# Kernel tuning notes

Measured on AMD Instinct MI355X. Metric: run time of the kernel, lower is better.

The kernel has to match this reference:

```python
import jax, jax.numpy as jnp
import numpy as np

N_NODES = 100000
N_EDGES = 3200000
IN_FEATS = 128
OUT_FEATS = 16
NEG_SLOPE = 0.2


def setup_inputs() -> dict:
    key = jax.random.key(0)
    k1, k2, k3, k4, k5, k6 = jax.random.split(key, 6)
    h = jax.random.normal(k1, (N_NODES, IN_FEATS), dtype=jnp.float32)
    src = jax.random.randint(k2, (N_EDGES,), 0, N_NODES, dtype=jnp.int64)
    dst = jax.random.randint(k3, (N_EDGES,), 0, N_NODES, dtype=jnp.int64)
    W = jax.random.normal(k4, (OUT_FEATS, IN_FEATS), dtype=jnp.float32) * (1.0 / np.sqrt(IN_FEATS))
    a_l = jax.random.normal(k5, (1, OUT_FEATS), dtype=jnp.float32) * (1.0 / np.sqrt(OUT_FEATS))
    a_r = jax.random.normal(k6, (1, OUT_FEATS), dtype=jnp.float32) * (1.0 / np.sqrt(OUT_FEATS))
    return {"h": h, "src": src, "dst": dst, "W": W, "a_l": a_l, "a_r": a_r}


def reference(h, src, dst, W, a_l, a_r):
    N = h.shape[0]
    # node projection: h @ fc.weight.T  -> [N, out]
    hW = h @ W.T
    # per-node attention logits: [N, 1]
    el = hW @ a_l.T
    er = hW @ a_r.T
    # u_add_v: per-edge logit e = el[src] + er[dst], then leaky_relu(0.2)
    e = jax.nn.leaky_relu(el[src] + er[dst], negative_slope=NEG_SLOPE)  # [E, 1]
    # edge_softmax over edges grouped by destination node (numerically stable)
    emax = jax.ops.segment_max(e, dst, num_segments=N)  # [N, 1], -inf for empty
    emax = jnp.where(jnp.isfinite(emax), emax, 0.0)
    e_exp = jnp.exp(e - emax[dst])
    esum = jax.ops.segment_sum(e_exp, dst, num_segments=N)  # [N, 1]
    alpha = e_exp / jnp.maximum(esum[dst], 1e-16)  # [E, 1]
    # u_mul_e + sum: weighted aggregation of source features at destinations
    out = jax.ops.segment_sum(hW[src] * alpha, dst, num_segments=N)  # [N, out]
    return out
```

## Files before the change

kernel.cpp:

```cpp
#include <hip/hip_runtime.h>
#include <hip/hip_bf16.h>
#include <stdint.h>

#define IN_F 128
#define OUT_F 16
#define NEG_SLOPE 0.2f
#define SB_BITS 9
#define SB_NODES 512
#define NBS 196
#define CAP_SB 17408
#define TILE_NODES 128
#define LCAP 4608
#define SC_E 8192
#define SB_SPACING 200

#define SMEM_BYTES (3136 + SC_E * 4)

__global__ __launch_bounds__(256) void proj_scatter_kernel(
    const float* __restrict__ h, const float* __restrict__ W,
    const float* __restrict__ a_l, const float* __restrict__ a_r,
    const int* __restrict__ src, const int* __restrict__ dst,
    __hip_bfloat16* __restrict__ hWbf, float* __restrict__ el,
    float* __restrict__ er, int* __restrict__ cursor,
    uint32_t* __restrict__ payload, int N, int E, int scatBlocks) {
  __shared__ __align__(16) uint8_t smem[SMEM_BYTES];
  int t = threadIdx.x;

  if ((int)blockIdx.x < scatBlocks) {
    int* hist = (int*)smem;
    int* pref = hist + NBS;
    int* gbase = pref + NBS;
    int* rank = gbase + NBS;
    uint32_t* sortedP = (uint32_t*)(smem + 3136);

    int start = blockIdx.x * SC_E;
    int end = min(E, start + SC_E);
    int cnt = end - start;

    if (t < NBS) { hist[t] = 0; rank[t] = 0; }
    __syncthreads();

    const int4* d4 = (const int4*)(dst + start);
    int n4 = cnt >> 2;
    for (int i = t; i < n4; i += 256) {
      int4 d = d4[i];
      atomicAdd(&hist[d.x >> SB_BITS], 1);
      atomicAdd(&hist[d.y >> SB_BITS], 1);
      atomicAdd(&hist[d.z >> SB_BITS], 1);
      atomicAdd(&hist[d.w >> SB_BITS], 1);
    }
    for (int i = start + (n4 << 2) + t; i < end; i += 256)
      atomicAdd(&hist[dst[i] >> SB_BITS], 1);
    __syncthreads();

    if (t < NBS) {
      int s = 0;
      for (int j = 0; j < t; ++j) s += hist[j];
      pref[t] = s;
      int c = hist[t];
      gbase[t] = c ? atomicAdd(&cursor[t * 16], c) : 0;
    }
    __syncthreads();

    const int4* s4 = (const int4*)(src + start);
    for (int i = t; i < n4; i += 256) {
      int4 d = d4[i];
      int4 s = s4[i];
#pragma unroll
      for (int j = 0; j < 4; ++j) {
        int dd = j == 0 ? d.x : j == 1 ? d.y : j == 2 ? d.z : d.w;
        int ss = j == 0 ? s.x : j == 1 ? s.y : j == 2 ? s.z : s.w;
        int b = dd >> SB_BITS;
        int r = atomicAdd(&rank[b], 1);
        sortedP[pref[b] + r] =
            ((uint32_t)ss << SB_BITS) | (uint32_t)(dd & (SB_NODES - 1));
      }
    }
    for (int i = start + (n4 << 2) + t; i < end; i += 256) {
      int dd = dst[i];
      int b = dd >> SB_BITS;
      int r = atomicAdd(&rank[b], 1);
      sortedP[pref[b] + r] =
          ((uint32_t)src[i] << SB_BITS) | (uint32_t)(dd & (SB_NODES - 1));
    }
    __syncthreads();

    int wv = t >> 6, ln = t & 63;
    for (int b = wv; b < NBS; b += 4) {
      int c = hist[b];
      int p0 = pref[b];
      size_t g0 = (size_t)b * CAP_SB + gbase[b];
      for (int j = ln; j < c; j += 64)
        if (gbase[b] + j < CAP_SB) payload[g0 + j] = sortedP[p0 + j];
    }
  } else {
    float* Ws = (float*)smem;
    for (int i = t; i < OUT_F * IN_F; i += 256) Ws[i] = W[i];
    __syncthreads();

    int node = ((int)blockIdx.x - scatBlocks) * 256 + t;
    if (node >= N) return;

    const float4* hrow = (const float4*)(h + (size_t)node * IN_F);
    float acc[OUT_F];
#pragma unroll
    for (int f = 0; f < OUT_F; ++f) acc[f] = 0.f;

#pragma unroll 4
    for (int k = 0; k < IN_F / 4; ++k) {
      float4 hv = hrow[k];
#pragma unroll
      for (int f = 0; f < OUT_F; ++f) {
        float4 wv = ((const float4*)(Ws + f * IN_F))[k];
        acc[f] += hv.x * wv.x + hv.y * wv.y + hv.z * wv.z + hv.w * wv.w;
      }
    }

    union {
      unsigned short us[OUT_F];
      uint4 q[2];
    } pk;
#pragma unroll
    for (int f = 0; f < OUT_F; ++f) {
      __hip_bfloat16 b = __float2bfloat16(acc[f]);
      pk.us[f] = *reinterpret_cast<unsigned short*>(&b);
    }
    uint4* dstq = (uint4*)(hWbf + (size_t)node * OUT_F);
    dstq[0] = pk.q[0];
    dstq[1] = pk.q[1];

    float vl = 0.f, vr = 0.f;
#pragma unroll
    for (int f = 0; f < OUT_F; ++f) {
      vl += acc[f] * a_l[f];
      vr += acc[f] * a_r[f];
    }
    el[node] = vl;
    er[node] = vr;
  }
}

__global__ __launch_bounds__(512) void agg_kernel(
    const uint32_t* __restrict__ payload, const int* __restrict__ cursor,
    const __hip_bfloat16* __restrict__ hWbf, const float* __restrict__ el,
    const float* __restrict__ er, float* __restrict__ out, int N) {
  __shared__ uint32_t sorted[LCAP];
  __shared__ float exS[LCAP];
  __shared__ int hist[TILE_NODES];
  __shared__ int pref[TILE_NODES];
  __shared__ int rank[TILE_NODES];
  __shared__ int kcnt;
  uint32_t* kept = (uint32_t*)exS;

  int t = threadIdx.x;
  int sb = blockIdx.x % SB_SPACING;
  uint32_t quad = blockIdx.x / SB_SPACING;
  if (sb >= NBS) return;
  size_t base = (size_t)sb * CAP_SB;
  int cnt = min(cursor[sb * 16], CAP_SB);

  if (t < TILE_NODES) { hist[t] = 0; rank[t] = 0; }
  if (t == 0) kcnt = 0;
  __syncthreads();

  const uint4* pay4 = (const uint4*)(payload + base);
  int n4 = (cnt + 3) >> 2;
  int lane = t & 63;
  for (int i = t; i < n4; i += 512) {
    uint4 v = pay4[i];
    int i0 = i << 2;
#pragma unroll
    for (int j = 0; j < 4; ++j) {
      uint32_t p = j == 0 ? v.x : j == 1 ? v.y : j == 2 ? v.z : v.w;
      bool keep = (i0 + j < cnt) && (((p >> 7) & 3u) == quad);
      unsigned long long m = __ballot(keep);
      if (m) {
        int leader = (int)(__ffsll((long long)m) - 1);
        int bbase = 0;
        if (lane == leader) bbase = atomicAdd(&kcnt, (int)__popcll(m));
        bbase = __shfl(bbase, leader);
        if (keep)
          kept[bbase + (int)__popcll(m & ((1ull << lane) - 1))] = p;
      }
    }
  }
  __syncthreads();
  int K = min(kcnt, LCAP);

  for (int i = t; i < K; i += 512)
    atomicAdd(&hist[kept[i] & (TILE_NODES - 1)], 1);
  __syncthreads();

  if (t < TILE_NODES) {
    int s = 0;
    for (int j = 0; j < t; ++j) s += hist[j];
    pref[t] = s;
  }
  __syncthreads();

  for (int i = t; i < K; i += 512) {
    uint32_t p = kept[i];
    int dl = (int)(p & (TILE_NODES - 1));
    int r = atomicAdd(&rank[dl], 1);
    sorted[pref[dl] + r] = p;
  }
  __syncthreads();

  int node0 = sb * SB_NODES + (int)quad * TILE_NODES;
  for (int i = t; i < K; i += 512) {
    uint32_t p = sorted[i];
    int s = (int)(p >> SB_BITS);
    float x = el[s] + er[node0 + (int)(p & (TILE_NODES - 1))];
    x = x > 0.f ? x : NEG_SLOPE * x;
    exS[i] = __expf(x);
  }
  __syncthreads();

  int g = t >> 4;
  int f = t & 15;
  for (int dl = g; dl < TILE_NODES; dl += 32) {
    int node = node0 + dl;
    if (node >= N) break;
    int k = pref[dl];
    int kend = k + hist[dl];
    float acc = 0.f;
    float es = 0.f;
#pragma unroll 4
    for (; k < kend; ++k) {
      float ex = exS[k];
      acc += ex * __bfloat162float(hWbf[(int)(sorted[k] >> SB_BITS) * OUT_F + f]);
      es += ex;
    }
    out[(size_t)node * OUT_F + f] = acc / fmaxf(es, 1e-16f);
  }
}

extern "C" void kernel_launch(void* const* d_in, const int* in_sizes, int n_in,
                              void* d_out, int out_size, void* d_ws, size_t ws_size,
                              hipStream_t stream) {
  const float* h   = (const float*)d_in[0];
  const int*   src = (const int*)d_in[1];
  const int*   dst = (const int*)d_in[2];
  const float* W   = (const float*)d_in[3];
  const float* a_l = (const float*)d_in[4];
  const float* a_r = (const float*)d_in[5];
  float* out = (float*)d_out;

  const int N = in_sizes[0] / IN_F;
  const int E = in_sizes[1];
  const int scatBlocks = (E + SC_E - 1) / SC_E;
  const int projBlocks = (N + 255) / 256;

  __hip_bfloat16* hWbf = (__hip_bfloat16*)d_ws;
  float* el = (float*)(hWbf + (size_t)N * OUT_F);
  float* er = el + N;
  int* cursor = (int*)(er + N);
  uint32_t* payload = (uint32_t*)(cursor + (size_t)NBS * 16);

  hipMemsetAsync(cursor, 0, (size_t)NBS * 16 * sizeof(int), stream);

  proj_scatter_kernel<<<scatBlocks + projBlocks, 256, 0, stream>>>(
      h, W, a_l, a_r, src, dst, hWbf, el, er, cursor, payload, N, E, scatBlocks);

  agg_kernel<<<SB_SPACING * 4, 512, 0, stream>>>(payload, cursor, hWbf, el, er,
                                                 out, N);
}
```

Before: 184.1 us.

## Bucket edges directly into 128-node tiles and vectorize aggregation gathers

The scatter pass now bins edges into 782 buckets of 128 destination nodes instead of 196 superbuckets of 512. Each aggregation block therefore reads only its own edges and no longer scans four times the payload with ballot-based filtering. The aggregation stage assigns 4 threads per node, each loading 4 bf16 features as a uint2 and writing a float4 output. The cost is more buckets in the scatter histogram and prefix scan (now two-level), smaller and more scattered payload write segments, and a fixed per-bucket capacity that could overflow on skewed inputs.

```diff
diff --git a/kernel.cpp b/kernel.cpp
--- a/kernel.cpp
+++ b/kernel.cpp
@@ -5,16 +5,19 @@
 #define IN_F 128
 #define OUT_F 16
 #define NEG_SLOPE 0.2f
-#define SB_BITS 9
-#define SB_NODES 512
-#define NBS 196
-#define CAP_SB 17408
-#define TILE_NODES 128
-#define LCAP 4608
+#define LB_BITS 7
+#define LB_NODES 128
+#define NB 782
+#define CAP 4608
 #define SC_E 8192
-#define SB_SPACING 200
-
-#define SMEM_BYTES (3136 + SC_E * 4)
+
+#define SMEM_BYTES (12512 + 1024 + SC_E * 4)
+
+__device__ __forceinline__ float u2f(uint32_t u) {
+  union { uint32_t i; float f; } c;
+  c.i = u;
+  return c.f;
+}
 
 __global__ __launch_bounds__(256) void proj_scatter_kernel(
     const float* __restrict__ h, const float* __restrict__ W,
@@ -28,37 +31,56 @@
 
   if ((int)blockIdx.x < scatBlocks) {
     int* hist = (int*)smem;
-    int* pref = hist + NBS;
-    int* gbase = pref + NBS;
-    int* rank = gbase + NBS;
-    uint32_t* sortedP = (uint32_t*)(smem + 3136);
+    int* pref = hist + NB;
+    int* gbase = pref + NB;
+    int* rank = gbase + NB;
+    int* tsum = rank + NB;
+    uint32_t* sortedP = (uint32_t*)(tsum + 256);
 
     int start = blockIdx.x * SC_E;
     int end = min(E, start + SC_E);
     int cnt = end - start;
 
-    if (t < NBS) { hist[t] = 0; rank[t] = 0; }
+    for (int i = t; i < NB; i += 256) { hist[i] = 0; rank[i] = 0; }
     __syncthreads();
 
     const int4* d4 = (const int4*)(dst + start);
     int n4 = cnt >> 2;
     for (int i = t; i < n4; i += 256) {
       int4 d = d4[i];
-      atomicAdd(&hist[d.x >> SB_BITS], 1);
-      atomicAdd(&hist[d.y >> SB_BITS], 1);
-      atomicAdd(&hist[d.z >> SB_BITS], 1);
-      atomicAdd(&hist[d.w >> SB_BITS], 1);
+      atomicAdd(&hist[d.x >> LB_BITS], 1);
+      atomicAdd(&hist[d.y >> LB_BITS], 1);
+      atomicAdd(&hist[d.z >> LB_BITS], 1);
+      atomicAdd(&hist[d.w >> LB_BITS], 1);
     }
     for (int i = start + (n4 << 2) + t; i < end; i += 256)
-      atomicAdd(&hist[dst[i] >> SB_BITS], 1);
-    __syncthreads();
-
-    if (t < NBS) {
-      int s = 0;
-      for (int j = 0; j < t; ++j) s += hist[j];
-      pref[t] = s;
-      int c = hist[t];
-      gbase[t] = c ? atomicAdd(&cursor[t * 16], c) : 0;
+      atomicAdd(&hist[dst[i] >> LB_BITS], 1);
+    __syncthreads();
+
+    {
+      int b0 = t * 4;
+      int s_loc = 0;
+      if (b0 < NB) {
+        int lim = min(b0 + 4, NB);
+        for (int j = b0; j < lim; ++j) s_loc += hist[j];
+      }
+      tsum[t] = s_loc;
+    }
+    __syncthreads();
+    {
+      int pre = 0;
+      for (int j = 0; j < t; ++j) pre += tsum[j];
+      int b0 = t * 4;
+      if (b0 < NB) {
+        int lim = min(b0 + 4, NB);
+        int run = pre;
+        for (int j = b0; j < lim; ++j) {
+          pref[j] = run;
+          int c = hist[j];
+          run += c;
+          gbase[j] = c ? atomicAdd(&cursor[j * 16], c) : 0;
+        }
+      }
     }
     __syncthreads();
 
@@ -70,28 +92,30 @@
       for (int j = 0; j < 4; ++j) {
         int dd = j == 0 ? d.x : j == 1 ? d.y : j == 2 ? d.z : d.w;
         int ss = j == 0 ? s.x : j == 1 ? s.y : j == 2 ? s.z : s.w;
-        int b = dd >> SB_BITS;
+        int b = dd >> LB_BITS;
         int r = atomicAdd(&rank[b], 1);
         sortedP[pref[b] + r] =
-            ((uint32_t)ss << SB_BITS) | (uint32_t)(dd & (SB_NODES - 1));
+            ((uint32_t)ss << LB_BITS) | (uint32_t)(dd & (LB_NODES - 1));
       }
     }
     for (int i = start + (n4 << 2) + t; i < end; i += 256) {
       int dd = dst[i];
-      int b = dd >> SB_BITS;
+      int b = dd >> LB_BITS;
       int r = atomicAdd(&rank[b], 1);
       sortedP[pref[b] + r] =
-          ((uint32_t)src[i] << SB_BITS) | (uint32_t)(dd & (SB_NODES - 1));
-    }
-    __syncthreads();
-
-    int wv = t >> 6, ln = t & 63;
-    for (int b = wv; b < NBS; b += 4) {
+          ((uint32_t)src[i] << LB_BITS) | (uint32_t)(dd & (LB_NODES - 1));
+    }
+    __syncthreads();
+
+    int g16 = t >> 4, l16 = t & 15;
+    for (int b = g16; b < NB; b += 16) {
       int c = hist[b];
+      if (c == 0) continue;
       int p0 = pref[b];
-      size_t g0 = (size_t)b * CAP_SB + gbase[b];
-      for (int j = ln; j < c; j += 64)
-        if (gbase[b] + j < CAP_SB) payload[g0 + j] = sortedP[p0 + j];
+      int gb = gbase[b];
+      size_t g0 = (size_t)b * CAP + (size_t)gb;
+      for (int j = l16; j < c; j += 16)
+        if (gb + j < CAP) payload[g0 + j] = sortedP[p0 + j];
     }
   } else {
     float* Ws = (float*)smem;
@@ -144,94 +168,80 @@
     const uint32_t* __restrict__ payload, const int* __restrict__ cursor,
     const __hip_bfloat16* __restrict__ hWbf, const float* __restrict__ el,
     const float* __restrict__ er, float* __restrict__ out, int N) {
-  __shared__ uint32_t sorted[LCAP];
-  __shared__ float exS[LCAP];
-  __shared__ int hist[TILE_NODES];
-  __shared__ int pref[TILE_NODES];
-  __shared__ int rank[TILE_NODES];
-  __shared__ int kcnt;
+  __shared__ __align__(16) uint32_t sorted[CAP];
+  __shared__ __align__(16) float exS[CAP];
+  __shared__ int hist[LB_NODES];
+  __shared__ int pref[LB_NODES];
+  __shared__ int rank[LB_NODES];
   uint32_t* kept = (uint32_t*)exS;
 
   int t = threadIdx.x;
-  int sb = blockIdx.x % SB_SPACING;
-  uint32_t quad = blockIdx.x / SB_SPACING;
-  if (sb >= NBS) return;
-  size_t base = (size_t)sb * CAP_SB;
-  int cnt = min(cursor[sb * 16], CAP_SB);
-
-  if (t < TILE_NODES) { hist[t] = 0; rank[t] = 0; }
-  if (t == 0) kcnt = 0;
+  int b = blockIdx.x;
+  size_t base = (size_t)b * CAP;
+  int cnt = min(cursor[b * 16], CAP);
+  int node0 = b << LB_BITS;
+
+  if (t < LB_NODES) { hist[t] = 0; rank[t] = 0; }
   __syncthreads();
 
   const uint4* pay4 = (const uint4*)(payload + base);
+  uint4* kept4 = (uint4*)kept;
   int n4 = (cnt + 3) >> 2;
-  int lane = t & 63;
   for (int i = t; i < n4; i += 512) {
     uint4 v = pay4[i];
+    kept4[i] = v;
     int i0 = i << 2;
-#pragma unroll
-    for (int j = 0; j < 4; ++j) {
-      uint32_t p = j == 0 ? v.x : j == 1 ? v.y : j == 2 ? v.z : v.w;
-      bool keep = (i0 + j < cnt) && (((p >> 7) & 3u) == quad);
-      unsigned long long m = __ballot(keep);
-      if (m) {
-        int leader = (int)(__ffsll((long long)m) - 1);
-        int bbase = 0;
-        if (lane == leader) bbase = atomicAdd(&kcnt, (int)__popcll(m));
-        bbase = __shfl(bbase, leader);
-        if (keep)
-          kept[bbase + (int)__popcll(m & ((1ull << lane) - 1))] = p;
-      }
-    }
-  }
-  __syncthreads();
-  int K = min(kcnt, LCAP);
-
-  for (int i = t; i < K; i += 512)
-    atomicAdd(&hist[kept[i] & (TILE_NODES - 1)], 1);
-  __syncthreads();
-
-  if (t < TILE_NODES) {
+    if (i0 + 0 < cnt) atomicAdd(&hist[v.x & (LB_NODES - 1)], 1);
+    if (i0 + 1 < cnt) atomicAdd(&hist[v.y & (LB_NODES - 1)], 1);
+    if (i0 + 2 < cnt) atomicAdd(&hist[v.z & (LB_NODES - 1)], 1);
+    if (i0 + 3 < cnt) atomicAdd(&hist[v.w & (LB_NODES - 1)], 1);
+  }
+  __syncthreads();
+
+  if (t < LB_NODES) {
     int s = 0;
     for (int j = 0; j < t; ++j) s += hist[j];
     pref[t] = s;
   }
   __syncthreads();
 
-  for (int i = t; i < K; i += 512) {
+  for (int i = t; i < cnt; i += 512) {
     uint32_t p = kept[i];
-    int dl = (int)(p & (TILE_NODES - 1));
+    int dl = (int)(p & (LB_NODES - 1));
     int r = atomicAdd(&rank[dl], 1);
     sorted[pref[dl] + r] = p;
   }
   __syncthreads();
 
-  int node0 = sb * SB_NODES + (int)quad * TILE_NODES;
-  for (int i = t; i < K; i += 512) {
+  for (int i = t; i < cnt; i += 512) {
     uint32_t p = sorted[i];
-    int s = (int)(p >> SB_BITS);
-    float x = el[s] + er[node0 + (int)(p & (TILE_NODES - 1))];
+    float x = el[p >> LB_BITS] + er[node0 + (int)(p & (LB_NODES - 1))];
     x = x > 0.f ? x : NEG_SLOPE * x;
     exS[i] = __expf(x);
   }
   __syncthreads();
 
-  int g = t >> 4;
-  int f = t & 15;
-  for (int dl = g; dl < TILE_NODES; dl += 32) {
-    int node = node0 + dl;
-    if (node >= N) break;
-    int k = pref[dl];
-    int kend = k + hist[dl];
-    float acc = 0.f;
-    float es = 0.f;
+  int g = t >> 2, f4 = t & 3;
+  int node = node0 + g;
+  if (node < N) {
+    int k = pref[g];
+    int kend = k + hist[g];
+    float a0 = 0.f, a1 = 0.f, a2 = 0.f, a3 = 0.f, es = 0.f;
+    const uint2* hw2 = (const uint2*)hWbf;
 #pragma unroll 4
     for (; k < kend; ++k) {
+      uint32_t p = sorted[k];
       float ex = exS[k];
-      acc += ex * __bfloat162float(hWbf[(int)(sorted[k] >> SB_BITS) * OUT_F + f]);
+      uint2 w = hw2[(size_t)(p >> LB_BITS) * 4 + f4];
+      a0 += ex * u2f(w.x << 16);
+      a1 += ex * u2f(w.x & 0xffff0000u);
+      a2 += ex * u2f(w.y << 16);
+      a3 += ex * u2f(w.y & 0xffff0000u);
       es += ex;
     }
-    out[(size_t)node * OUT_F + f] = acc / fmaxf(es, 1e-16f);
+    float inv = 1.0f / fmaxf(es, 1e-16f);
+    float4 o = make_float4(a0 * inv, a1 * inv, a2 * inv, a3 * inv);
+    ((float4*)(out + (size_t)node * OUT_F))[f4] = o;
   }
 }
 
@@ -255,13 +265,12 @@
   float* el = (float*)(hWbf + (size_t)N * OUT_F);
   float* er = el + N;
   int* cursor = (int*)(er + N);
-  uint32_t* payload = (uint32_t*)(cursor + (size_t)NBS * 16);
-
-  hipMemsetAsync(cursor, 0, (size_t)NBS * 16 * sizeof(int), stream);
+  uint32_t* payload = (uint32_t*)(cursor + (size_t)NB * 16);
+
+  hipMemsetAsync(cursor, 0, (size_t)NB * 16 * sizeof(int), stream);
 
   proj_scatter_kernel<<<scatBlocks + projBlocks, 256, 0, stream>>>(
       h, W, a_l, a_r, src, dst, hWbf, el, er, cursor, payload, N, E, scatBlocks);
 
-  agg_kernel<<<SB_SPACING * 4, 512, 0, stream>>>(payload, cursor, hWbf, el, er,
-                                                 out, N);
-}
+  agg_kernel<<<NB, 512, 0, stream>>>(payload, cursor, hWbf, el, er, out, N);
+}
```

After: 180.9 us. No clear change (-1.8%).
